# Kernel tuning notes

Hardware: AMD Instinct MI355X
Metric: run time of the kernel (lower is better)

## Reference

```python
import jax, jax.numpy as jnp
import numpy as np

N_BATTERS = 5000
N_PITCHERS = 2000
N_PAIRS = 10_000_000


def setup_inputs() -> dict:
    key = jax.random.key(0)
    k1, k2, k3, k4, k5, k6, k7 = jax.random.split(key, 7)
    v1 = jax.random.normal(k1, (N_BATTERS,), dtype=jnp.float32)
    v2 = jax.random.normal(k2, (N_PITCHERS,), dtype=jnp.float32)
    weight = jax.random.uniform(k3, (1,), dtype=jnp.float32)
    event1 = jax.random.uniform(k4, (N_PAIRS,), dtype=jnp.float32)
    event2 = jax.random.uniform(k5, (N_PAIRS,), dtype=jnp.float32)
    batter_idx = jax.random.randint(k6, (N_PAIRS,), 0, N_BATTERS, dtype=jnp.int32)
    pitcher_idx = jax.random.randint(k7, (N_PAIRS,), 0, N_PITCHERS, dtype=jnp.int32)
    return {
        "v1": v1,
        "v2": v2,
        "weight": weight,
        "event1": event1,
        "event2": event2,
        "batter_idx": batter_idx,
        "pitcher_idx": pitcher_idx,
    }


def reference(v1, v2, weight, event1, event2, batter_idx, pitcher_idx):
    # gather per-pair player strengths
    b = v1[batter_idx]            # [N]
    p = v2[pitcher_idx]           # [N]
    w = weight[0]
    z = w * b + (1.0 - w) * p     # logit per pair
    # temp/(1+temp) with temp=exp(z) == sigmoid(z)
    prob = jax.nn.sigmoid(z)
    prob = jnp.clip(prob, 1e-06, 0.999999)
    ll = jnp.sum(event1 * jnp.log(prob) + event2 * jnp.log1p(-prob))
    return ll
```

## Files before the change

### kernel.cpp

```cpp
#include <hip/hip_runtime.h>

#define BLOCK 256
#define GRID  1280
#define NB_MAX 5000
#define NP_MAX 2000

__global__ __launch_bounds__(BLOCK) void vs_ll_kernel(
    const float* __restrict__ v1, const float* __restrict__ v2,
    const float* __restrict__ weight,
    const float* __restrict__ e1, const float* __restrict__ e2,
    const int*  __restrict__ bidx, const int* __restrict__ pidx,
    int nb, int np, int n, float* __restrict__ partials)
{
    __shared__ float s_v1[NB_MAX];
    __shared__ float s_v2[NP_MAX];
    __shared__ float s_red[BLOCK / 64];

    for (int i = threadIdx.x; i < nb; i += BLOCK) s_v1[i] = v1[i];
    for (int i = threadIdx.x; i < np; i += BLOCK) s_v2[i] = v2[i];
    __syncthreads();

    const float w     = weight[0];
    const float onemw = 1.0f - w;
    const float LOG_LO = -13.815511f;
    const float LOG_HI = -1.0000005e-6f;

    float acc = 0.0f;

    const int n4     = n >> 2;
    const int gid    = blockIdx.x * BLOCK + threadIdx.x;
    const int stride = GRID * BLOCK;
    const float4* e1v = (const float4*)e1;
    const float4* e2v = (const float4*)e2;
    const int4*   bv  = (const int4*)bidx;
    const int4*   pv  = (const int4*)pidx;

    for (int i = gid; i < n4; i += stride) {
        float4 a = e1v[i];
        float4 c = e2v[i];
        int4   b = bv[i];
        int4   p = pv[i];

        float bb[4] = { s_v1[b.x], s_v1[b.y], s_v1[b.z], s_v1[b.w] };
        float pp[4] = { s_v2[p.x], s_v2[p.y], s_v2[p.z], s_v2[p.w] };
        float u1[4] = { a.x, a.y, a.z, a.w };
        float u2[4] = { c.x, c.y, c.z, c.w };

        #pragma unroll
        for (int j = 0; j < 4; ++j) {
            float z  = fmaf(w, bb[j], onemw * pp[j]);
            float az = fabsf(z);
            float l  = __logf(1.0f + __expf(-az));
            float logp = -(fmaxf(-z, 0.0f) + l);
            float logq = -(fmaxf( z, 0.0f) + l);
            logp = fminf(fmaxf(logp, LOG_LO), LOG_HI);
            logq = fminf(fmaxf(logq, LOG_LO), LOG_HI);
            acc = fmaf(u1[j], logp, acc);
            acc = fmaf(u2[j], logq, acc);
        }
    }

    for (int i = (n4 << 2) + gid; i < n; i += stride) {
        float z  = fmaf(w, s_v1[bidx[i]], onemw * s_v2[pidx[i]]);
        float az = fabsf(z);
        float l  = __logf(1.0f + __expf(-az));
        float logp = fminf(fmaxf(-(fmaxf(-z, 0.0f) + l), LOG_LO), LOG_HI);
        float logq = fminf(fmaxf(-(fmaxf( z, 0.0f) + l), LOG_LO), LOG_HI);
        acc = fmaf(e1[i], logp, acc);
        acc = fmaf(e2[i], logq, acc);
    }

    #pragma unroll
    for (int off = 32; off > 0; off >>= 1)
        acc += __shfl_down(acc, off, 64);

    const int lane = threadIdx.x & 63;
    const int wid  = threadIdx.x >> 6;
    if (lane == 0) s_red[wid] = acc;
    __syncthreads();
    if (threadIdx.x == 0) {
        float t = 0.0f;
        #pragma unroll
        for (int k = 0; k < BLOCK / 64; ++k) t += s_red[k];
        partials[blockIdx.x] = t;
    }
}

__global__ __launch_bounds__(BLOCK) void vs_reduce_kernel(
    const float* __restrict__ partials, int nparts, float* __restrict__ out)
{
    __shared__ float s_red[BLOCK / 64];
    float acc = 0.0f;
    for (int i = threadIdx.x; i < nparts; i += BLOCK) acc += partials[i];
    #pragma unroll
    for (int off = 32; off > 0; off >>= 1)
        acc += __shfl_down(acc, off, 64);
    const int lane = threadIdx.x & 63;
    const int wid  = threadIdx.x >> 6;
    if (lane == 0) s_red[wid] = acc;
    __syncthreads();
    if (threadIdx.x == 0) {
        float t = 0.0f;
        #pragma unroll
        for (int k = 0; k < BLOCK / 64; ++k) t += s_red[k];
        out[0] = t;
    }
}

extern "C" void kernel_launch(void* const* d_in, const int* in_sizes, int n_in,
                              void* d_out, int out_size, void* d_ws, size_t ws_size,
                              hipStream_t stream) {
    const float* v1     = (const float*)d_in[0];
    const float* v2     = (const float*)d_in[1];
    const float* weight = (const float*)d_in[2];
    const float* e1     = (const float*)d_in[3];
    const float* e2     = (const float*)d_in[4];
    const int*   bidx   = (const int*)d_in[5];
    const int*   pidx   = (const int*)d_in[6];

    const int nb = in_sizes[0];
    const int np = in_sizes[1];
    const int n  = in_sizes[3];

    float* partials = (float*)d_ws;
    float* out      = (float*)d_out;

    vs_ll_kernel<<<GRID, BLOCK, 0, stream>>>(v1, v2, weight, e1, e2, bidx, pidx,
                                             nb, np, n, partials);
    vs_reduce_kernel<<<1, BLOCK, 0, stream>>>(partials, GRID, out);
}
```

Baseline: 36.11 us.

## Software-prefetch next grid-stride iteration and enlarge blocks to 512 threads

Restructures the grid-stride loop so the next iteration's four vector loads are issued before the current iteration's shared-memory gathers and transcendental math, overlapping global memory latency with compute. Block size goes to 512 with a launch-bounds occupancy hint and the grid shrinks to 1024 blocks, which means fewer per-block shared-table fills. The reduce kernel is pinned to 256 threads so it no longer depends on BLOCK. Prefetching doubles the live vector registers and may limit occupancy.

```diff
diff --git a/kernel.cpp b/kernel.cpp
--- a/kernel.cpp
+++ b/kernel.cpp
@@ -1,11 +1,11 @@
 #include <hip/hip_runtime.h>
 
-#define BLOCK 256
-#define GRID  1280
+#define BLOCK 512
+#define GRID  1024
 #define NB_MAX 5000
 #define NP_MAX 2000
 
-__global__ __launch_bounds__(BLOCK) void vs_ll_kernel(
+__global__ __launch_bounds__(BLOCK, 8) void vs_ll_kernel(
     const float* __restrict__ v1, const float* __restrict__ v2,
     const float* __restrict__ weight,
     const float* __restrict__ e1, const float* __restrict__ e2,
@@ -35,11 +35,16 @@
     const int4*   bv  = (const int4*)bidx;
     const int4*   pv  = (const int4*)pidx;
 
-    for (int i = gid; i < n4; i += stride) {
-        float4 a = e1v[i];
-        float4 c = e2v[i];
-        int4   b = bv[i];
-        int4   p = pv[i];
+    int  i     = gid;
+    bool valid = (i < n4);
+    float4 a, c; int4 b, p;
+    if (valid) { a = e1v[i]; c = e2v[i]; b = bv[i]; p = pv[i]; }
+
+    while (valid) {
+        const int  inext = i + stride;
+        const bool vnext = (inext < n4);
+        float4 a2, c2; int4 b2, p2;
+        if (vnext) { a2 = e1v[inext]; c2 = e2v[inext]; b2 = bv[inext]; p2 = pv[inext]; }
 
         float bb[4] = { s_v1[b.x], s_v1[b.y], s_v1[b.z], s_v1[b.w] };
         float pp[4] = { s_v2[p.x], s_v2[p.y], s_v2[p.z], s_v2[p.w] };
@@ -58,16 +63,19 @@
             acc = fmaf(u1[j], logp, acc);
             acc = fmaf(u2[j], logq, acc);
         }
+
+        a = a2; c = c2; b = b2; p = p2;
+        i = inext; valid = vnext;
     }
 
-    for (int i = (n4 << 2) + gid; i < n; i += stride) {
-        float z  = fmaf(w, s_v1[bidx[i]], onemw * s_v2[pidx[i]]);
+    for (int t = (n4 << 2) + gid; t < n; t += stride) {
+        float z  = fmaf(w, s_v1[bidx[t]], onemw * s_v2[pidx[t]]);
         float az = fabsf(z);
         float l  = __logf(1.0f + __expf(-az));
         float logp = fminf(fmaxf(-(fmaxf(-z, 0.0f) + l), LOG_LO), LOG_HI);
         float logq = fminf(fmaxf(-(fmaxf( z, 0.0f) + l), LOG_LO), LOG_HI);
-        acc = fmaf(e1[i], logp, acc);
-        acc = fmaf(e2[i], logq, acc);
+        acc = fmaf(e1[t], logp, acc);
+        acc = fmaf(e2[t], logq, acc);
     }
 
     #pragma unroll
@@ -86,12 +94,12 @@
     }
 }
 
-__global__ __launch_bounds__(BLOCK) void vs_reduce_kernel(
+__global__ __launch_bounds__(256) void vs_reduce_kernel(
     const float* __restrict__ partials, int nparts, float* __restrict__ out)
 {
-    __shared__ float s_red[BLOCK / 64];
+    __shared__ float s_red[4];
     float acc = 0.0f;
-    for (int i = threadIdx.x; i < nparts; i += BLOCK) acc += partials[i];
+    for (int i = threadIdx.x; i < nparts; i += 256) acc += partials[i];
     #pragma unroll
     for (int off = 32; off > 0; off >>= 1)
         acc += __shfl_down(acc, off, 64);
@@ -102,7 +110,7 @@
     if (threadIdx.x == 0) {
         float t = 0.0f;
         #pragma unroll
-        for (int k = 0; k < BLOCK / 64; ++k) t += s_red[k];
+        for (int k = 0; k < 4; ++k) t += s_red[k];
         out[0] = t;
     }
 }
@@ -127,5 +135,5 @@
 
     vs_ll_kernel<<<GRID, BLOCK, 0, stream>>>(v1, v2, weight, e1, e2, bidx, pidx,
                                              nb, np, n, partials);
-    vs_reduce_kernel<<<1, BLOCK, 0, stream>>>(partials, GRID, out);
+    vs_reduce_kernel<<<1, 256, 0, stream>>>(partials, GRID, out);
 }
```

Measured after the change: 34.19 us. 1.06x faster.
